# Performance work log

Hardware: AMD Instinct MI355X
Metric: run time of the kernel (lower is better)

The kernel has to match this reference:

```python
import jax, jax.numpy as jnp
import numpy as np

N, M, D, O = 16384, 4096, 256, 256

def setup_inputs() -> dict:
    key = jax.random.key(0)
    k1, k2, k3, k4, k5, k6, k7 = jax.random.split(key, 7)
    H_fine = jax.random.normal(k1, (N, D), dtype=jnp.float32)
    H_coarse = jax.random.normal(k2, (M, D), dtype=jnp.float32)
    inter_channel_adj = jax.random.randint(k3, (N, M), 0, 2).astype(jnp.float32)
    # attention = nn.Linear(2D, 1): weight vector [2D], bias scalar
    wa = jax.random.normal(k4, (2 * D,), dtype=jnp.float32) * (1.0 / np.sqrt(2 * D))
    ba = jax.random.normal(k5, (1,), dtype=jnp.float32) * 0.01
    # transform = nn.Linear(D, O), xavier_uniform weight
    lim = np.sqrt(6.0 / (D + O)).astype(np.float32)
    Wt = jax.random.uniform(k6, (O, D), minval=-lim, maxval=lim, dtype=jnp.float32)
    bt = jax.random.normal(k7, (O,), dtype=jnp.float32) * 0.01
    return {"H_fine": H_fine, "H_coarse": H_coarse,
            "inter_channel_adj": inter_channel_adj,
            "wa": wa, "ba": ba, "Wt": Wt, "bt": bt}

def reference(H_fine, H_coarse, inter_channel_adj, wa, ba, Wt, bt):
    d = H_fine.shape[-1]
    # additive attention: score_ij = [hf_i ; hc_j] . wa + b
    # = hf_i . wa[:d] + hc_j . wa[d:] + b  (avoids [N,M,2D] concat)
    sf = H_fine @ wa[:d]            # [N]
    sc = H_coarse @ wa[d:]          # [M]
    scores = sf[:, None] + sc[None, :] + ba[0]        # [N, M]
    masked = scores * inter_channel_adj               # [N, M]
    weights = jax.nn.softmax(masked, axis=-1)         # [N, M]
    attn_out = weights @ H_coarse                     # [N, D]
    attn_out = attn_out + H_fine                      # add_self=True
    out = attn_out @ Wt.T + bt                        # [N, O]
    return jax.nn.relu(out)
```

## Files before the change

### kernel.cpp

```cpp
#include <hip/hip_runtime.h>
#include <hip/hip_bf16.h>
#include <stdint.h>

#define N_ 16384
#define M_ 4096
#define D_ 256
#define O_ 256

#define WS_T    0
#define WS_U    65536
#define WS_R    81920
#define WS_LSUM 98304
#define WS_WTP  163840
#define WS_BP   294912
#define WS_ABM  2457600
#define WS_CP   10846208

typedef float  f32x4  __attribute__((ext_vector_type(4)));
typedef short  short8 __attribute__((ext_vector_type(8)));
typedef unsigned short ushortx4 __attribute__((ext_vector_type(4)));

__device__ __forceinline__ unsigned short f2bf(float f) {
  uint32_t u = __float_as_uint(f);
  u += 0x7FFFu + ((u >> 16) & 1u);
  return (unsigned short)(u >> 16);
}
__device__ __forceinline__ uint32_t cvtpk(float a, float b) {
  __hip_bfloat162 h = __float22bfloat162_rn(float2{a, b});
  uint32_t u;
  __builtin_memcpy(&u, &h, 4);
  return u;
}
__device__ __forceinline__ float bf2f(unsigned short v) {
  return __uint_as_float((uint32_t)v << 16);
}

__global__ __launch_bounds__(256) void rowdot_exp_kernel(
    const float* __restrict__ X, const float* __restrict__ w,
    const float* __restrict__ bias, float* __restrict__ outv) {
  int wv = threadIdx.x >> 6, lane = threadIdx.x & 63;
  int row = blockIdx.x * 4 + wv;
  const float4* x4 = (const float4*)(X + (size_t)row * D_);
  const float4* w4 = (const float4*)w;
  float4 xa = x4[lane], wa4 = w4[lane];
  float s = xa.x * wa4.x + xa.y * wa4.y + xa.z * wa4.z + xa.w * wa4.w;
#pragma unroll
  for (int off = 32; off > 0; off >>= 1) s += __shfl_xor(s, off);
  if (lane == 0) outv[row] = expf(s + (bias ? bias[0] : 0.0f));
}

__global__ __launch_bounds__(256) void hc_pack_kernel(
    const float* __restrict__ Hc, unsigned short* __restrict__ BP,
    float* __restrict__ R) {
  __shared__ float tile[64][65];
  __shared__ float red[4][64];
  int bk = blockIdx.x >> 2;
  int bc = blockIdx.x & 3;
  int k0 = bk * 64, col0 = bc * 64;
  int t = threadIdx.x;
  int lane = t & 63, wv = t >> 6;
  int m = lane & 15, q = lane >> 4;
  float colsum = 0.0f;
#pragma unroll
  for (int i = 0; i < 16; ++i) {
    int e = t + 256 * i;
    int kk = e >> 6, cc = e & 63;
    float v = Hc[(size_t)(k0 + kk) * D_ + col0 + cc];
    tile[kk][cc] = v;
    colsum += v;
  }
  red[wv][t & 63] = colsum;
  __syncthreads();
  if (t < 64)
    atomicAdd(&R[col0 + t], red[0][t] + red[1][t] + red[2][t] + red[3][t]);
#pragma unroll
  for (int t8 = 0; t8 < 2; ++t8) {
    int tile_id = t8 * 4 + wv;
    int sub = tile_id >> 2, g = tile_id & 3;
    int kgg = bk * 2 + sub;
    int cgg = bc * 4 + g;
    short8 v8;
#pragma unroll
    for (int j = 0; j < 8; ++j)
      v8[j] = (short)f2bf(tile[sub * 32 + q * 8 + j][g * 16 + m]);
    *(short8*)(BP + ((size_t)(kgg * 16 + cgg) * 64 + lane) * 8) = v8;
  }
}

__global__ __launch_bounds__(256) void wt_pack_kernel(
    const float* __restrict__ Wt, unsigned short* __restrict__ WtP) {
  int t = blockIdx.x * 256 + threadIdx.x;
  int lane = t & 63, cg = (t >> 6) & 15, kg = t >> 10;
  int m = lane & 15, q = lane >> 4;
  const float* src = Wt + (size_t)(cg * 16 + m) * D_ + kg * 32 + q * 8;
  float4 w0 = *(const float4*)src, w1 = *(const float4*)(src + 4);
  short8 v8;
  v8[0] = (short)f2bf(w0.x); v8[1] = (short)f2bf(w0.y);
  v8[2] = (short)f2bf(w0.z); v8[3] = (short)f2bf(w0.w);
  v8[4] = (short)f2bf(w1.x); v8[5] = (short)f2bf(w1.y);
  v8[6] = (short)f2bf(w1.z); v8[7] = (short)f2bf(w1.w);
  *(short8*)(WtP + (size_t)t * 8) = v8;
}

__global__ __launch_bounds__(256) void pack_bits_kernel(
    const float* __restrict__ adj, const float* __restrict__ tv,
    const float* __restrict__ uv, unsigned long long* __restrict__ ABM,
    float* __restrict__ Lsum) {
  __shared__ float u_lds[M_];
  int tid = threadIdx.x;
  int w = tid >> 6, lane = tid & 63;
  for (int i = tid; i < M_; i += 256) u_lds[i] = uv[i];
  __syncthreads();
  int r0 = (blockIdx.x * 4 + w) * 2;
  const float* arA = adj + (size_t)r0 * M_;
  const float* arB = arA + M_;
  float suA = 0.f, scA = 0.f, suB = 0.f, scB = 0.f;

  float a0 = arA[lane], a1 = arA[64 + lane], a2 = arA[128 + lane], a3 = arA[192 + lane];
  float b0 = arB[lane], b1 = arB[64 + lane], b2 = arB[128 + lane], b3 = arB[192 + lane];
#pragma unroll 1
  for (int i = 0; i < 16; ++i) {
    int k0 = i * 256;
    int k1 = (i + 1 < 16) ? k0 + 256 : 0;
    float na0 = arA[k1 + lane],       na1 = arA[k1 + 64 + lane];
    float na2 = arA[k1 + 128 + lane], na3 = arA[k1 + 192 + lane];
    float nb0 = arB[k1 + lane],       nb1 = arB[k1 + 64 + lane];
    float nb2 = arB[k1 + 128 + lane], nb3 = arB[k1 + 192 + lane];

    unsigned long long wA0 = __ballot(a0 != 0.0f), wA1 = __ballot(a1 != 0.0f);
    unsigned long long wA2 = __ballot(a2 != 0.0f), wA3 = __ballot(a3 != 0.0f);
    unsigned long long wB0 = __ballot(b0 != 0.0f), wB1 = __ballot(b1 != 0.0f);
    unsigned long long wB2 = __ballot(b2 != 0.0f), wB3 = __ballot(b3 != 0.0f);
    suA = fmaf(a0, u_lds[k0 + lane], suA);
    suA = fmaf(a1, u_lds[k0 + 64 + lane], suA);
    suA = fmaf(a2, u_lds[k0 + 128 + lane], suA);
    suA = fmaf(a3, u_lds[k0 + 192 + lane], suA);
    scA += (a0 + a1) + (a2 + a3);
    suB = fmaf(b0, u_lds[k0 + lane], suB);
    suB = fmaf(b1, u_lds[k0 + 64 + lane], suB);
    suB = fmaf(b2, u_lds[k0 + 128 + lane], suB);
    suB = fmaf(b3, u_lds[k0 + 192 + lane], suB);
    scB += (b0 + b1) + (b2 + b3);
    if (lane < 8) {
      int sel = lane & 3;
      unsigned long long vA = sel == 0 ? wA0 : sel == 1 ? wA1 : sel == 2 ? wA2 : wA3;
      unsigned long long vB = sel == 0 ? wB0 : sel == 1 ? wB1 : sel == 2 ? wB2 : wB3;
      int r = (lane < 4) ? r0 : r0 + 1;
      ABM[(size_t)r * 64 + i * 4 + sel] = (lane < 4) ? vA : vB;
    }
    a0 = na0; a1 = na1; a2 = na2; a3 = na3;
    b0 = nb0; b1 = nb1; b2 = nb2; b3 = nb3;
  }
#pragma unroll
  for (int off = 32; off > 0; off >>= 1) {
    suA += __shfl_xor(suA, off); scA += __shfl_xor(scA, off);
    suB += __shfl_xor(suB, off); scB += __shfl_xor(scB, off);
  }
  if (lane == 0) {
    Lsum[r0] = tv[r0] * suA - scA;
    Lsum[r0 + 1] = tv[r0 + 1] * suB - scB;
  }
}

__device__ __forceinline__ short8 frag_bits(uint32_t bits, float t,
                                            float4 u0, float4 u1) {
  float c[8];
  c[0] = fmaf(t, u0.x, -1.0f); c[1] = fmaf(t, u0.y, -1.0f);
  c[2] = fmaf(t, u0.z, -1.0f); c[3] = fmaf(t, u0.w, -1.0f);
  c[4] = fmaf(t, u1.x, -1.0f); c[5] = fmaf(t, u1.y, -1.0f);
  c[6] = fmaf(t, u1.z, -1.0f); c[7] = fmaf(t, u1.w, -1.0f);
  union { short8 s; uint32_t u[4]; } r;
#pragma unroll
  for (int p = 0; p < 4; ++p) {
    uint32_t mlo = 0u - ((bits >> (2 * p)) & 1u);
    uint32_t mhi = 0u - ((bits >> (2 * p + 1)) & 1u);
    r.u[p] = cvtpk(c[2 * p], c[2 * p + 1]) &
             ((mlo & 0x0000FFFFu) | (mhi & 0xFFFF0000u));
  }
  return r.s;
}

__global__ __launch_bounds__(1024, 4) void gemm_kernel(
    const unsigned int* __restrict__ ABM32, const unsigned short* __restrict__ BP,
    const float* __restrict__ tv, const float* __restrict__ uv,
    unsigned short* __restrict__ Cp) {
  __shared__ unsigned int bt2[64][129];
  __shared__ float u_lds[M_];
  int tid = threadIdx.x;
  int w = tid >> 6, lane = tid & 63;
  int q = lane >> 4, m = lane & 15;
  int colq = w >> 2, ksub = w & 3;
  int i0 = blockIdx.x * 64;

  const unsigned short* bbase = BP + (size_t)(colq * 4) * 512 + (size_t)lane * 8;
  int kg0 = ksub * 32;
  short8 curB[4];
#pragma unroll
  for (int n = 0; n < 4; ++n)
    curB[n] = *(const short8*)(bbase + ((size_t)kg0 * 16 + n) * 512);
  float t0 = tv[i0 + m], t1 = tv[i0 + 16 + m];
  float t2 = tv[i0 + 32 + m], t3 = tv[i0 + 48 + m];

  for (int i = tid; i < M_; i += 1024) u_lds[i] = uv[i];
  for (int p = tid; p < 8192; p += 1024) {
    int row = p >> 7, word = p & 127;
    bt2[row][word] = ABM32[(size_t)(i0 + row) * 128 + word];
  }

  f32x4 acc[4][4];
#pragma unroll
  for (int s = 0; s < 4; ++s)
#pragma unroll
    for (int n = 0; n < 4; ++n) acc[s][n] = (f32x4){0.f, 0.f, 0.f, 0.f};

  __syncthreads();

  for (int it = 0; it < 32; ++it) {
    int kg = kg0 + it;
    int kn = (it + 1 < 32) ? kg + 1 : kg0;
    short8 nB[4];
#pragma unroll
    for (int n = 0; n < 4; ++n)
      nB[n] = *(const short8*)(bbase + ((size_t)kn * 16 + n) * 512);

    float4 u0 = *(const float4*)&u_lds[kg * 32 + q * 8];
    float4 u1 = *(const float4*)&u_lds[kg * 32 + q * 8 + 4];
    uint32_t b0 = bt2[m][kg],      b1 = bt2[16 + m][kg];
    uint32_t b2 = bt2[32 + m][kg], b3 = bt2[48 + m][kg];
    int sh = q * 8;
    short8 af0 = frag_bits((b0 >> sh) & 0xffu, t0, u0, u1);
    short8 af1 = frag_bits((b1 >> sh) & 0xffu, t1, u0, u1);
    short8 af2 = frag_bits((b2 >> sh) & 0xffu, t2, u0, u1);
    short8 af3 = frag_bits((b3 >> sh) & 0xffu, t3, u0, u1);
#pragma unroll
    for (int n = 0; n < 4; ++n) {
      acc[0][n] = __builtin_amdgcn_mfma_f32_16x16x32_bf16(af0, curB[n], acc[0][n], 0, 0, 0);
      acc[1][n] = __builtin_amdgcn_mfma_f32_16x16x32_bf16(af1, curB[n], acc[1][n], 0, 0, 0);
      acc[2][n] = __builtin_amdgcn_mfma_f32_16x16x32_bf16(af2, curB[n], acc[2][n], 0, 0, 0);
      acc[3][n] = __builtin_amdgcn_mfma_f32_16x16x32_bf16(af3, curB[n], acc[3][n], 0, 0, 0);
    }
#pragma unroll
    for (int n = 0; n < 4; ++n) curB[n] = nB[n];
  }

  unsigned short* cpb = Cp + (size_t)ksub * N_ * D_;
#pragma unroll
  for (int s = 0; s < 4; ++s)
#pragma unroll
    for (int n = 0; n < 4; ++n) {
      int col = colq * 64 + n * 16 + m;
#pragma unroll
      for (int r = 0; r < 4; ++r) {
        size_t row = (size_t)i0 + s * 16 + q * 4 + r;
        cpb[row * D_ + col] = f2bf(acc[s][n][r]);
      }
    }
}

__global__ __launch_bounds__(256, 4) void epilogue_kernel(
    const unsigned short* __restrict__ Cp, const float* __restrict__ Lsum,
    const float* __restrict__ Rv, const float* __restrict__ Hf,
    const unsigned short* __restrict__ WtP, const float* __restrict__ bt,
    float* __restrict__ out) {
  __shared__ alignas(16) unsigned short attn[32][264];
  int tid = threadIdx.x;
  int w = tid >> 6, lane = tid & 63;
  int rtile = w & 1, chalf = w >> 1;
  int q = lane >> 4, m = lane & 15;
  int i0 = blockIdx.x * 32;

  float4 rv = *(const float4*)(Rv + lane * 4);
#pragma unroll
  for (int rr = 0; rr < 8; ++rr) {
    int r = w * 8 + rr;
    size_t row = (size_t)i0 + r;
    float invL = 1.0f / (Lsum[row] + (float)M_);
    ushortx4 c0 = *(const ushortx4*)(Cp + row * D_ + lane * 4);
    ushortx4 c1 = *(const ushortx4*)(Cp + ((size_t)N_ + row) * D_ + lane * 4);
    ushortx4 c2 = *(const ushortx4*)(Cp + ((size_t)2 * N_ + row) * D_ + lane * 4);
    ushortx4 c3 = *(const ushortx4*)(Cp + ((size_t)3 * N_ + row) * D_ + lane * 4);
    float4 hv = *(const float4*)(Hf + row * D_ + lane * 4);
    float s0 = (bf2f(c0[0]) + bf2f(c1[0])) + (bf2f(c2[0]) + bf2f(c3[0]));
    float s1 = (bf2f(c0[1]) + bf2f(c1[1])) + (bf2f(c2[1]) + bf2f(c3[1]));
    float s2 = (bf2f(c0[2]) + bf2f(c1[2])) + (bf2f(c2[2]) + bf2f(c3[2]));
    float s3 = (bf2f(c0[3]) + bf2f(c1[3])) + (bf2f(c2[3]) + bf2f(c3[3]));
    attn[r][lane * 4 + 0] = f2bf(fmaf(s0 + rv.x, invL, hv.x));
    attn[r][lane * 4 + 1] = f2bf(fmaf(s1 + rv.y, invL, hv.y));
    attn[r][lane * 4 + 2] = f2bf(fmaf(s2 + rv.z, invL, hv.z));
    attn[r][lane * 4 + 3] = f2bf(fmaf(s3 + rv.w, invL, hv.w));
  }
  __syncthreads();

  f32x4 facc[8];
#pragma unroll
  for (int n = 0; n < 8; ++n) facc[n] = (f32x4){0.f, 0.f, 0.f, 0.f};
  const unsigned short* wwave = WtP + (size_t)chalf * 4096 + (size_t)lane * 8;
#pragma unroll
  for (int kf = 0; kf < 8; ++kf) {
    short8 af = *(const short8*)&attn[rtile * 16 + m][kf * 32 + q * 8];
#pragma unroll
    for (int n = 0; n < 8; ++n) {
      short8 bf = *(const short8*)(wwave + ((size_t)kf * 16 + n) * 512);
      facc[n] = __builtin_amdgcn_mfma_f32_16x16x32_bf16(af, bf, facc[n], 0, 0, 0);
    }
  }
#pragma unroll
  for (int n = 0; n < 8; ++n) {
    int col = chalf * 128 + n * 16 + m;
    float b = bt[col];
#pragma unroll
    for (int r = 0; r < 4; ++r) {
      size_t row = (size_t)i0 + rtile * 16 + q * 4 + r;
      out[row * O_ + col] = fmaxf(facc[n][r] + b, 0.0f);
    }
  }
}

extern "C" void kernel_launch(void* const* d_in, const int* in_sizes, int n_in,
                              void* d_out, int out_size, void* d_ws, size_t ws_size,
                              hipStream_t stream) {
  const float* Hf  = (const float*)d_in[0];
  const float* Hc  = (const float*)d_in[1];
  const float* adj = (const float*)d_in[2];
  const float* wa  = (const float*)d_in[3];
  const float* ba  = (const float*)d_in[4];
  const float* Wt  = (const float*)d_in[5];
  const float* bt  = (const float*)d_in[6];
  float* out = (float*)d_out;

  char* ws = (char*)d_ws;
  float* tv   = (float*)(ws + WS_T);
  float* uv   = (float*)(ws + WS_U);
  float* Rv   = (float*)(ws + WS_R);
  float* Lsum = (float*)(ws + WS_LSUM);
  unsigned short* WtP = (unsigned short*)(ws + WS_WTP);
  unsigned short* BP  = (unsigned short*)(ws + WS_BP);
  unsigned long long* ABM = (unsigned long long*)(ws + WS_ABM);
  unsigned short* Cp  = (unsigned short*)(ws + WS_CP);

  hipMemsetAsync(Rv, 0, D_ * sizeof(float), stream);

  rowdot_exp_kernel<<<N_ / 4, 256, 0, stream>>>(Hf, wa, ba, tv);
  rowdot_exp_kernel<<<M_ / 4, 256, 0, stream>>>(Hc, wa + D_, nullptr, uv);
  hc_pack_kernel<<<256, 256, 0, stream>>>(Hc, BP, Rv);
  wt_pack_kernel<<<32, 256, 0, stream>>>(Wt, WtP);

  pack_bits_kernel<<<2048, 256, 0, stream>>>(adj, tv, uv, ABM, Lsum);
  gemm_kernel<<<N_ / 64, 1024, 0, stream>>>((const unsigned int*)ABM, BP, tv, uv, Cp);
  epilogue_kernel<<<N_ / 32, 256, 0, stream>>>(Cp, Lsum, Rv, Hf, WtP, bt, out);
}
```

Measured before the change: 487.8 us.

## Factor masked exp-weight GEMM into two bf16 GEMMs with pre-scaled coarse operand

The (t_i*u_j - 1)*mask weight is split algebraically into t_i*mask @ (u*Hc) plus -mask @ Hc. A-fragments are now built from bitmasks and constants alone, with no per-element FMA or bf16 conversion. Two packed B operands are precomputed in hc_pack, and the work split changes from 4 k-slices by 4 column quarters to 2 k-slices by 8 column groups. Partial sums are kept in fp32, so the epilogue reads only two partials. This doubles MFMA count and B-operand traffic in exchange for removing the VALU fragment build, and rounding t and u*Hc to bf16 separately may change accuracy.

```diff
diff --git a/kernel.cpp b/kernel.cpp
--- a/kernel.cpp
+++ b/kernel.cpp
@@ -12,13 +12,13 @@
 #define WS_R    81920
 #define WS_LSUM 98304
 #define WS_WTP  163840
-#define WS_BP   294912
-#define WS_ABM  2457600
-#define WS_CP   10846208
+#define WS_BP1  294912
+#define WS_BP2  2392064
+#define WS_ABM  4489216
+#define WS_CP   12877824
 
 typedef float  f32x4  __attribute__((ext_vector_type(4)));
 typedef short  short8 __attribute__((ext_vector_type(8)));
-typedef unsigned short ushortx4 __attribute__((ext_vector_type(4)));
 
 __device__ __forceinline__ unsigned short f2bf(float f) {
   uint32_t u = __float_as_uint(f);
@@ -30,9 +30,6 @@
   uint32_t u;
   __builtin_memcpy(&u, &h, 4);
   return u;
-}
-__device__ __forceinline__ float bf2f(unsigned short v) {
-  return __uint_as_float((uint32_t)v << 16);
 }
 
 __global__ __launch_bounds__(256) void rowdot_exp_kernel(
@@ -50,16 +47,19 @@
 }
 
 __global__ __launch_bounds__(256) void hc_pack_kernel(
-    const float* __restrict__ Hc, unsigned short* __restrict__ BP,
+    const float* __restrict__ Hc, const float* __restrict__ uv,
+    unsigned short* __restrict__ BP1, unsigned short* __restrict__ BP2,
     float* __restrict__ R) {
   __shared__ float tile[64][65];
   __shared__ float red[4][64];
+  __shared__ float u_tile[64];
   int bk = blockIdx.x >> 2;
   int bc = blockIdx.x & 3;
   int k0 = bk * 64, col0 = bc * 64;
   int t = threadIdx.x;
   int lane = t & 63, wv = t >> 6;
   int m = lane & 15, q = lane >> 4;
+  if (t < 64) u_tile[t] = uv[k0 + t];
   float colsum = 0.0f;
 #pragma unroll
   for (int i = 0; i < 16; ++i) {
@@ -79,11 +79,17 @@
     int sub = tile_id >> 2, g = tile_id & 3;
     int kgg = bk * 2 + sub;
     int cgg = bc * 4 + g;
-    short8 v8;
-#pragma unroll
-    for (int j = 0; j < 8; ++j)
-      v8[j] = (short)f2bf(tile[sub * 32 + q * 8 + j][g * 16 + m]);
-    *(short8*)(BP + ((size_t)(kgg * 16 + cgg) * 64 + lane) * 8) = v8;
+    short8 v1, v2;
+#pragma unroll
+    for (int j = 0; j < 8; ++j) {
+      int kk = sub * 32 + q * 8 + j;
+      float v = tile[kk][g * 16 + m];
+      v2[j] = (short)f2bf(v);
+      v1[j] = (short)f2bf(u_tile[kk] * v);
+    }
+    size_t off = ((size_t)(kgg * 16 + cgg) * 64 + lane) * 8;
+    *(short8*)(BP1 + off) = v1;
+    *(short8*)(BP2 + off) = v2;
   }
 }
 
@@ -162,103 +168,108 @@
   }
 }
 
-__device__ __forceinline__ short8 frag_bits(uint32_t bits, float t,
-                                            float4 u0, float4 u1) {
-  float c[8];
-  c[0] = fmaf(t, u0.x, -1.0f); c[1] = fmaf(t, u0.y, -1.0f);
-  c[2] = fmaf(t, u0.z, -1.0f); c[3] = fmaf(t, u0.w, -1.0f);
-  c[4] = fmaf(t, u1.x, -1.0f); c[5] = fmaf(t, u1.y, -1.0f);
-  c[6] = fmaf(t, u1.z, -1.0f); c[7] = fmaf(t, u1.w, -1.0f);
-  union { short8 s; uint32_t u[4]; } r;
+__device__ __forceinline__ void frag01(uint32_t bits, uint32_t tpk,
+                                       short8* a1, short8* a2) {
+  union { short8 s; uint32_t u[4]; } r1, r2;
 #pragma unroll
   for (int p = 0; p < 4; ++p) {
     uint32_t mlo = 0u - ((bits >> (2 * p)) & 1u);
     uint32_t mhi = 0u - ((bits >> (2 * p + 1)) & 1u);
-    r.u[p] = cvtpk(c[2 * p], c[2 * p + 1]) &
-             ((mlo & 0x0000FFFFu) | (mhi & 0xFFFF0000u));
-  }
-  return r.s;
+    uint32_t msk = (mlo & 0x0000FFFFu) | (mhi & 0xFFFF0000u);
+    r1.u[p] = tpk & msk;
+    r2.u[p] = 0xBF80BF80u & msk;
+  }
+  *a1 = r1.s; *a2 = r2.s;
 }
 
 __global__ __launch_bounds__(1024, 4) void gemm_kernel(
-    const unsigned int* __restrict__ ABM32, const unsigned short* __restrict__ BP,
-    const float* __restrict__ tv, const float* __restrict__ uv,
-    unsigned short* __restrict__ Cp) {
+    const unsigned int* __restrict__ ABM32, const unsigned short* __restrict__ BP1,
+    const unsigned short* __restrict__ BP2, const float* __restrict__ tv,
+    float* __restrict__ Cp) {
   __shared__ unsigned int bt2[64][129];
-  __shared__ float u_lds[M_];
   int tid = threadIdx.x;
   int w = tid >> 6, lane = tid & 63;
   int q = lane >> 4, m = lane & 15;
-  int colq = w >> 2, ksub = w & 3;
+  int colq = w & 7, ksub = w >> 3;
   int i0 = blockIdx.x * 64;
 
-  const unsigned short* bbase = BP + (size_t)(colq * 4) * 512 + (size_t)lane * 8;
-  int kg0 = ksub * 32;
-  short8 curB[4];
-#pragma unroll
-  for (int n = 0; n < 4; ++n)
-    curB[n] = *(const short8*)(bbase + ((size_t)kg0 * 16 + n) * 512);
-  float t0 = tv[i0 + m], t1 = tv[i0 + 16 + m];
+  float t0 = tv[i0 + m],      t1 = tv[i0 + 16 + m];
   float t2 = tv[i0 + 32 + m], t3 = tv[i0 + 48 + m];
-
-  for (int i = tid; i < M_; i += 1024) u_lds[i] = uv[i];
+  uint32_t tp0 = cvtpk(t0, t0), tp1 = cvtpk(t1, t1);
+  uint32_t tp2 = cvtpk(t2, t2), tp3 = cvtpk(t3, t3);
+
   for (int p = tid; p < 8192; p += 1024) {
     int row = p >> 7, word = p & 127;
     bt2[row][word] = ABM32[(size_t)(i0 + row) * 128 + word];
   }
 
-  f32x4 acc[4][4];
+  f32x4 acc[4][2];
 #pragma unroll
   for (int s = 0; s < 4; ++s)
 #pragma unroll
-    for (int n = 0; n < 4; ++n) acc[s][n] = (f32x4){0.f, 0.f, 0.f, 0.f};
+    for (int n = 0; n < 2; ++n) acc[s][n] = (f32x4){0.f, 0.f, 0.f, 0.f};
+
+  int kg0 = ksub * 64;
+  const unsigned short* b1p = BP1 + (size_t)(kg0 * 16 + colq * 2) * 512 + (size_t)lane * 8;
+  const unsigned short* b2p = BP2 + (size_t)(kg0 * 16 + colq * 2) * 512 + (size_t)lane * 8;
+  int sh = q * 8;
 
   __syncthreads();
 
-  for (int it = 0; it < 32; ++it) {
+#pragma unroll 2
+  for (int it = 0; it < 64; ++it) {
     int kg = kg0 + it;
-    int kn = (it + 1 < 32) ? kg + 1 : kg0;
-    short8 nB[4];
-#pragma unroll
-    for (int n = 0; n < 4; ++n)
-      nB[n] = *(const short8*)(bbase + ((size_t)kn * 16 + n) * 512);
-
-    float4 u0 = *(const float4*)&u_lds[kg * 32 + q * 8];
-    float4 u1 = *(const float4*)&u_lds[kg * 32 + q * 8 + 4];
-    uint32_t b0 = bt2[m][kg],      b1 = bt2[16 + m][kg];
-    uint32_t b2 = bt2[32 + m][kg], b3 = bt2[48 + m][kg];
-    int sh = q * 8;
-    short8 af0 = frag_bits((b0 >> sh) & 0xffu, t0, u0, u1);
-    short8 af1 = frag_bits((b1 >> sh) & 0xffu, t1, u0, u1);
-    short8 af2 = frag_bits((b2 >> sh) & 0xffu, t2, u0, u1);
-    short8 af3 = frag_bits((b3 >> sh) & 0xffu, t3, u0, u1);
-#pragma unroll
-    for (int n = 0; n < 4; ++n) {
-      acc[0][n] = __builtin_amdgcn_mfma_f32_16x16x32_bf16(af0, curB[n], acc[0][n], 0, 0, 0);
-      acc[1][n] = __builtin_amdgcn_mfma_f32_16x16x32_bf16(af1, curB[n], acc[1][n], 0, 0, 0);
-      acc[2][n] = __builtin_amdgcn_mfma_f32_16x16x32_bf16(af2, curB[n], acc[2][n], 0, 0, 0);
-      acc[3][n] = __builtin_amdgcn_mfma_f32_16x16x32_bf16(af3, curB[n], acc[3][n], 0, 0, 0);
-    }
-#pragma unroll
-    for (int n = 0; n < 4; ++n) curB[n] = nB[n];
-  }
-
-  unsigned short* cpb = Cp + (size_t)ksub * N_ * D_;
+    const unsigned short* b1k = b1p + (size_t)it * 8192;
+    const unsigned short* b2k = b2p + (size_t)it * 8192;
+    short8 B1a = *(const short8*)(b1k);
+    short8 B1b = *(const short8*)(b1k + 512);
+    short8 B2a = *(const short8*)(b2k);
+    short8 B2b = *(const short8*)(b2k + 512);
+
+    uint32_t w0 = (bt2[m][kg] >> sh) & 0xffu;
+    uint32_t w1 = (bt2[16 + m][kg] >> sh) & 0xffu;
+    uint32_t w2 = (bt2[32 + m][kg] >> sh) & 0xffu;
+    uint32_t w3 = (bt2[48 + m][kg] >> sh) & 0xffu;
+
+    short8 a1, a2;
+    frag01(w0, tp0, &a1, &a2);
+    acc[0][0] = __builtin_amdgcn_mfma_f32_16x16x32_bf16(a1, B1a, acc[0][0], 0, 0, 0);
+    acc[0][0] = __builtin_amdgcn_mfma_f32_16x16x32_bf16(a2, B2a, acc[0][0], 0, 0, 0);
+    acc[0][1] = __builtin_amdgcn_mfma_f32_16x16x32_bf16(a1, B1b, acc[0][1], 0, 0, 0);
+    acc[0][1] = __builtin_amdgcn_mfma_f32_16x16x32_bf16(a2, B2b, acc[0][1], 0, 0, 0);
+    frag01(w1, tp1, &a1, &a2);
+    acc[1][0] = __builtin_amdgcn_mfma_f32_16x16x32_bf16(a1, B1a, acc[1][0], 0, 0, 0);
+    acc[1][0] = __builtin_amdgcn_mfma_f32_16x16x32_bf16(a2, B2a, acc[1][0], 0, 0, 0);
+    acc[1][1] = __builtin_amdgcn_mfma_f32_16x16x32_bf16(a1, B1b, acc[1][1], 0, 0, 0);
+    acc[1][1] = __builtin_amdgcn_mfma_f32_16x16x32_bf16(a2, B2b, acc[1][1], 0, 0, 0);
+    frag01(w2, tp2, &a1, &a2);
+    acc[2][0] = __builtin_amdgcn_mfma_f32_16x16x32_bf16(a1, B1a, acc[2][0], 0, 0, 0);
+    acc[2][0] = __builtin_amdgcn_mfma_f32_16x16x32_bf16(a2, B2a, acc[2][0], 0, 0, 0);
+    acc[2][1] = __builtin_amdgcn_mfma_f32_16x16x32_bf16(a1, B1b, acc[2][1], 0, 0, 0);
+    acc[2][1] = __builtin_amdgcn_mfma_f32_16x16x32_bf16(a2, B2b, acc[2][1], 0, 0, 0);
+    frag01(w3, tp3, &a1, &a2);
+    acc[3][0] = __builtin_amdgcn_mfma_f32_16x16x32_bf16(a1, B1a, acc[3][0], 0, 0, 0);
+    acc[3][0] = __builtin_amdgcn_mfma_f32_16x16x32_bf16(a2, B2a, acc[3][0], 0, 0, 0);
+    acc[3][1] = __builtin_amdgcn_mfma_f32_16x16x32_bf16(a1, B1b, acc[3][1], 0, 0, 0);
+    acc[3][1] = __builtin_amdgcn_mfma_f32_16x16x32_bf16(a2, B2b, acc[3][1], 0, 0, 0);
+  }
+
+  float* cpb = Cp + (size_t)ksub * N_ * D_;
 #pragma unroll
   for (int s = 0; s < 4; ++s)
 #pragma unroll
-    for (int n = 0; n < 4; ++n) {
-      int col = colq * 64 + n * 16 + m;
+    for (int n = 0; n < 2; ++n) {
+      int col = (colq * 2 + n) * 16 + m;
 #pragma unroll
       for (int r = 0; r < 4; ++r) {
         size_t row = (size_t)i0 + s * 16 + q * 4 + r;
-        cpb[row * D_ + col] = f2bf(acc[s][n][r]);
+        cpb[row * D_ + col] = acc[s][n][r];
       }
     }
 }
 
 __global__ __launch_bounds__(256, 4) void epilogue_kernel(
-    const unsigned short* __restrict__ Cp, const float* __restrict__ Lsum,
+    const float* __restrict__ Cp, const float* __restrict__ Lsum,
     const float* __restrict__ Rv, const float* __restrict__ Hf,
     const unsigned short* __restrict__ WtP, const float* __restrict__ bt,
     float* __restrict__ out) {
@@ -275,19 +286,13 @@
     int r = w * 8 + rr;
     size_t row = (size_t)i0 + r;
     float invL = 1.0f / (Lsum[row] + (float)M_);
-    ushortx4 c0 = *(const ushortx4*)(Cp + row * D_ + lane * 4);
-    ushortx4 c1 = *(const ushortx4*)(Cp + ((size_t)N_ + row) * D_ + lane * 4);
-    ushortx4 c2 = *(const ushortx4*)(Cp + ((size_t)2 * N_ + row) * D_ + lane * 4);
-    ushortx4 c3 = *(const ushortx4*)(Cp + ((size_t)3 * N_ + row) * D_ + lane * 4);
+    float4 c0 = *(const float4*)(Cp + row * D_ + lane * 4);
+    float4 c1 = *(const float4*)(Cp + ((size_t)N_ + row) * D_ + lane * 4);
     float4 hv = *(const float4*)(Hf + row * D_ + lane * 4);
-    float s0 = (bf2f(c0[0]) + bf2f(c1[0])) + (bf2f(c2[0]) + bf2f(c3[0]));
-    float s1 = (bf2f(c0[1]) + bf2f(c1[1])) + (bf2f(c2[1]) + bf2f(c3[1]));
-    float s2 = (bf2f(c0[2]) + bf2f(c1[2])) + (bf2f(c2[2]) + bf2f(c3[2]));
-    float s3 = (bf2f(c0[3]) + bf2f(c1[3])) + (bf2f(c2[3]) + bf2f(c3[3]));
-    attn[r][lane * 4 + 0] = f2bf(fmaf(s0 + rv.x, invL, hv.x));
-    attn[r][lane * 4 + 1] = f2bf(fmaf(s1 + rv.y, invL, hv.y));
-    attn[r][lane * 4 + 2] = f2bf(fmaf(s2 + rv.z, invL, hv.z));
-    attn[r][lane * 4 + 3] = f2bf(fmaf(s3 + rv.w, invL, hv.w));
+    attn[r][lane * 4 + 0] = f2bf(fmaf(c0.x + c1.x + rv.x, invL, hv.x));
+    attn[r][lane * 4 + 1] = f2bf(fmaf(c0.y + c1.y + rv.y, invL, hv.y));
+    attn[r][lane * 4 + 2] = f2bf(fmaf(c0.z + c1.z + rv.z, invL, hv.z));
+    attn[r][lane * 4 + 3] = f2bf(fmaf(c0.w + c1.w + rv.w, invL, hv.w));
   }
   __syncthreads();
 
@@ -334,18 +339,19 @@
   float* Rv   = (float*)(ws + WS_R);
   float* Lsum = (float*)(ws + WS_LSUM);
   unsigned short* WtP = (unsigned short*)(ws + WS_WTP);
-  unsigned short* BP  = (unsigned short*)(ws + WS_BP);
+  unsigned short* BP1 = (unsigned short*)(ws + WS_BP1);
+  unsigned short* BP2 = (unsigned short*)(ws + WS_BP2);
   unsigned long long* ABM = (unsigned long long*)(ws + WS_ABM);
-  unsigned short* Cp  = (unsigned short*)(ws + WS_CP);
+  float* Cp = (float*)(ws + WS_CP);
 
   hipMemsetAsync(Rv, 0, D_ * sizeof(float), stream);
 
   rowdot_exp_kernel<<<N_ / 4, 256, 0, stream>>>(Hf, wa, ba, tv);
   rowdot_exp_kernel<<<M_ / 4, 256, 0, stream>>>(Hc, wa + D_, nullptr, uv);
-  hc_pack_kernel<<<256, 256, 0, stream>>>(Hc, BP, Rv);
+  hc_pack_kernel<<<256, 256, 0, stream>>>(Hc, uv, BP1, BP2, Rv);
   wt_pack_kernel<<<32, 256, 0, stream>>>(Wt, WtP);
 
   pack_bits_kernel<<<2048, 256, 0, stream>>>(adj, tv, uv, ABM, Lsum);
-  gemm_kernel<<<N_ / 64, 1024, 0, stream>>>((const unsigned int*)ABM, BP, tv, uv, Cp);
+  gemm_kernel<<<N_ / 64, 1024, 0, stream>>>((const unsigned int*)ABM, BP1, BP2, tv, Cp);
   epilogue_kernel<<<N_ / 32, 256, 0, stream>>>(Cp, Lsum, Rv, Hf, WtP, bt, out);
 }
```

New measurement: 509.8 us. +4.5%, slower.

## Fuse GEMM with epilogue via LDS split-K reduction and merge prep kernels

Applied to the files above, without the earlier changes.

Merges the four small preprocessing kernels into a single prep launch that dispatches on block index. Fuses the epilogue into the main GEMM kernel: the four k-split partial accumulators are reduced in shared memory instead of being written to and reread from a bf16 global buffer. The block then applies normalization, the residual and the second MFMA GEMM in place. This removes about 32 MB of intermediate global traffic and two launches, but raises LDS usage to about 115 KB per block and adds serialized reduction barriers, which may lower occupancy.

```diff
diff --git a/kernel.cpp b/kernel.cpp
--- a/kernel.cpp
+++ b/kernel.cpp
@@ -13,12 +13,10 @@
 #define WS_LSUM 98304
 #define WS_WTP  163840
 #define WS_BP   294912
-#define WS_ABM  2457600
-#define WS_CP   10846208
+#define WS_ABM  2392064
 
 typedef float  f32x4  __attribute__((ext_vector_type(4)));
 typedef short  short8 __attribute__((ext_vector_type(8)));
-typedef unsigned short ushortx4 __attribute__((ext_vector_type(4)));
 
 __device__ __forceinline__ unsigned short f2bf(float f) {
   uint32_t u = __float_as_uint(f);
@@ -31,75 +29,74 @@
   __builtin_memcpy(&u, &h, 4);
   return u;
 }
-__device__ __forceinline__ float bf2f(unsigned short v) {
-  return __uint_as_float((uint32_t)v << 16);
-}
-
-__global__ __launch_bounds__(256) void rowdot_exp_kernel(
-    const float* __restrict__ X, const float* __restrict__ w,
-    const float* __restrict__ bias, float* __restrict__ outv) {
-  int wv = threadIdx.x >> 6, lane = threadIdx.x & 63;
-  int row = blockIdx.x * 4 + wv;
-  const float4* x4 = (const float4*)(X + (size_t)row * D_);
-  const float4* w4 = (const float4*)w;
-  float4 xa = x4[lane], wa4 = w4[lane];
-  float s = xa.x * wa4.x + xa.y * wa4.y + xa.z * wa4.z + xa.w * wa4.w;
-#pragma unroll
-  for (int off = 32; off > 0; off >>= 1) s += __shfl_xor(s, off);
-  if (lane == 0) outv[row] = expf(s + (bias ? bias[0] : 0.0f));
-}
-
-__global__ __launch_bounds__(256) void hc_pack_kernel(
-    const float* __restrict__ Hc, unsigned short* __restrict__ BP,
-    float* __restrict__ R) {
+
+__global__ __launch_bounds__(256) void prep_kernel(
+    const float* __restrict__ Hf, const float* __restrict__ Hc,
+    const float* __restrict__ wa, const float* __restrict__ ba,
+    const float* __restrict__ Wt, float* __restrict__ tv,
+    float* __restrict__ uv, unsigned short* __restrict__ BP,
+    unsigned short* __restrict__ WtP, float* __restrict__ Rv) {
   __shared__ float tile[64][65];
   __shared__ float red[4][64];
-  int bk = blockIdx.x >> 2;
-  int bc = blockIdx.x & 3;
-  int k0 = bk * 64, col0 = bc * 64;
+  int b = blockIdx.x;
   int t = threadIdx.x;
-  int lane = t & 63, wv = t >> 6;
-  int m = lane & 15, q = lane >> 4;
-  float colsum = 0.0f;
-#pragma unroll
-  for (int i = 0; i < 16; ++i) {
-    int e = t + 256 * i;
-    int kk = e >> 6, cc = e & 63;
-    float v = Hc[(size_t)(k0 + kk) * D_ + col0 + cc];
-    tile[kk][cc] = v;
-    colsum += v;
-  }
-  red[wv][t & 63] = colsum;
-  __syncthreads();
-  if (t < 64)
-    atomicAdd(&R[col0 + t], red[0][t] + red[1][t] + red[2][t] + red[3][t]);
-#pragma unroll
-  for (int t8 = 0; t8 < 2; ++t8) {
-    int tile_id = t8 * 4 + wv;
-    int sub = tile_id >> 2, g = tile_id & 3;
-    int kgg = bk * 2 + sub;
-    int cgg = bc * 4 + g;
+  if (b < 5120) {
+    int wv = t >> 6, lane = t & 63;
+    const float* X; const float* w; const float* bias; float* outv; int row;
+    if (b < 4096) { X = Hf; w = wa;      bias = ba;      outv = tv; row = b * 4 + wv; }
+    else          { X = Hc; w = wa + D_; bias = nullptr; outv = uv; row = (b - 4096) * 4 + wv; }
+    const float4* x4 = (const float4*)(X + (size_t)row * D_);
+    const float4* w4 = (const float4*)w;
+    float4 xa = x4[lane], wa4 = w4[lane];
+    float s = xa.x * wa4.x + xa.y * wa4.y + xa.z * wa4.z + xa.w * wa4.w;
+#pragma unroll
+    for (int off = 32; off > 0; off >>= 1) s += __shfl_xor(s, off);
+    if (lane == 0) outv[row] = expf(s + (bias ? bias[0] : 0.0f));
+  } else if (b < 5376) {
+    int bb = b - 5120;
+    int bk = bb >> 2;
+    int bc = bb & 3;
+    int k0 = bk * 64, col0 = bc * 64;
+    int lane = t & 63, wv = t >> 6;
+    int m = lane & 15, q = lane >> 4;
+    float colsum = 0.0f;
+#pragma unroll
+    for (int i = 0; i < 16; ++i) {
+      int e = t + 256 * i;
+      int kk = e >> 6, cc = e & 63;
+      float v = Hc[(size_t)(k0 + kk) * D_ + col0 + cc];
+      tile[kk][cc] = v;
+      colsum += v;
+    }
+    red[wv][t & 63] = colsum;
+    __syncthreads();
+    if (t < 64)
+      atomicAdd(&Rv[col0 + t], red[0][t] + red[1][t] + red[2][t] + red[3][t]);
+#pragma unroll
+    for (int t8 = 0; t8 < 2; ++t8) {
+      int tile_id = t8 * 4 + wv;
+      int sub = tile_id >> 2, g = tile_id & 3;
+      int kgg = bk * 2 + sub;
+      int cgg = bc * 4 + g;
+      short8 v8;
+#pragma unroll
+      for (int j = 0; j < 8; ++j)
+        v8[j] = (short)f2bf(tile[sub * 32 + q * 8 + j][g * 16 + m]);
+      *(short8*)(BP + ((size_t)(kgg * 16 + cgg) * 64 + lane) * 8) = v8;
+    }
+  } else {
+    int tt = (b - 5376) * 256 + t;
+    int lane = tt & 63, cg = (tt >> 6) & 15, kg = tt >> 10;
+    int m = lane & 15, q = lane >> 4;
+    const float* src = Wt + (size_t)(cg * 16 + m) * D_ + kg * 32 + q * 8;
+    float4 w0 = *(const float4*)src, w1 = *(const float4*)(src + 4);
     short8 v8;
-#pragma unroll
-    for (int j = 0; j < 8; ++j)
-      v8[j] = (short)f2bf(tile[sub * 32 + q * 8 + j][g * 16 + m]);
-    *(short8*)(BP + ((size_t)(kgg * 16 + cgg) * 64 + lane) * 8) = v8;
-  }
-}
-
-__global__ __launch_bounds__(256) void wt_pack_kernel(
-    const float* __restrict__ Wt, unsigned short* __restrict__ WtP) {
-  int t = blockIdx.x * 256 + threadIdx.x;
-  int lane = t & 63, cg = (t >> 6) & 15, kg = t >> 10;
-  int m = lane & 15, q = lane >> 4;
-  const float* src = Wt + (size_t)(cg * 16 + m) * D_ + kg * 32 + q * 8;
-  float4 w0 = *(const float4*)src, w1 = *(const float4*)(src + 4);
-  short8 v8;
-  v8[0] = (short)f2bf(w0.x); v8[1] = (short)f2bf(w0.y);
-  v8[2] = (short)f2bf(w0.z); v8[3] = (short)f2bf(w0.w);
-  v8[4] = (short)f2bf(w1.x); v8[5] = (short)f2bf(w1.y);
-  v8[6] = (short)f2bf(w1.z); v8[7] = (short)f2bf(w1.w);
-  *(short8*)(WtP + (size_t)t * 8) = v8;
+    v8[0] = (short)f2bf(w0.x); v8[1] = (short)f2bf(w0.y);
+    v8[2] = (short)f2bf(w0.z); v8[3] = (short)f2bf(w0.w);
+    v8[4] = (short)f2bf(w1.x); v8[5] = (short)f2bf(w1.y);
+    v8[6] = (short)f2bf(w1.z); v8[7] = (short)f2bf(w1.w);
+    *(short8*)(WtP + (size_t)tt * 8) = v8;
+  }
 }
 
 __global__ __launch_bounds__(256) void pack_bits_kernel(
@@ -180,12 +177,18 @@
   return r.s;
 }
 
-__global__ __launch_bounds__(1024, 4) void gemm_kernel(
+__global__ __launch_bounds__(1024, 4) void mega_kernel(
     const unsigned int* __restrict__ ABM32, const unsigned short* __restrict__ BP,
     const float* __restrict__ tv, const float* __restrict__ uv,
-    unsigned short* __restrict__ Cp) {
-  __shared__ unsigned int bt2[64][129];
-  __shared__ float u_lds[M_];
+    const float* __restrict__ Lsum, const float* __restrict__ Rv,
+    const float* __restrict__ Hf, const unsigned short* __restrict__ WtP,
+    const float* __restrict__ bt, float* __restrict__ out) {
+  __shared__ __align__(16) char smem[114944];
+  unsigned int (*bt2)[129] = (unsigned int (*)[129])(smem);
+  float* u_lds = (float*)(smem + 33024);
+  float (*Cred)[256] = (float (*)[256])(smem + 49408);
+  unsigned short (*attn)[264] = (unsigned short (*)[264])(smem);
+
   int tid = threadIdx.x;
   int w = tid >> 6, lane = tid & 63;
   int q = lane >> 4, m = lane & 15;
@@ -243,75 +246,72 @@
     for (int n = 0; n < 4; ++n) curB[n] = nB[n];
   }
 
-  unsigned short* cpb = Cp + (size_t)ksub * N_ * D_;
-#pragma unroll
-  for (int s = 0; s < 4; ++s)
+#pragma unroll
+  for (int s4 = 0; s4 < 4; ++s4) {
+    if (ksub == s4) {
+#pragma unroll
+      for (int s = 0; s < 4; ++s)
+#pragma unroll
+        for (int n = 0; n < 4; ++n) {
+          int col = colq * 64 + n * 16 + m;
+#pragma unroll
+          for (int r = 0; r < 4; ++r) {
+            int rl = s * 16 + q * 4 + r;
+            if (s4 == 0) Cred[rl][col] = acc[s][n][r];
+            else         Cred[rl][col] += acc[s][n][r];
+          }
+        }
+    }
+    __syncthreads();
+  }
+
+  {
+    int row = tid >> 4;
+    int c0 = (tid & 15) * 16;
+    size_t grow = (size_t)i0 + row;
+    float invL = 1.0f / (Lsum[grow] + (float)M_);
+    const float* hfp = Hf + grow * D_ + c0;
+    const float* rvp = Rv + c0;
+    const float* crp = &Cred[row][c0];
+#pragma unroll
+    for (int g = 0; g < 4; ++g) {
+      float4 cv = *(const float4*)(crp + g * 4);
+      float4 rv = *(const float4*)(rvp + g * 4);
+      float4 hv = *(const float4*)(hfp + g * 4);
+      float v0 = fmaf(cv.x + rv.x, invL, hv.x);
+      float v1 = fmaf(cv.y + rv.y, invL, hv.y);
+      float v2 = fmaf(cv.z + rv.z, invL, hv.z);
+      float v3 = fmaf(cv.w + rv.w, invL, hv.w);
+      *(uint32_t*)&attn[row][c0 + g * 4]     = cvtpk(v0, v1);
+      *(uint32_t*)&attn[row][c0 + g * 4 + 2] = cvtpk(v2, v3);
+    }
+  }
+  __syncthreads();
+
+  {
+    int rt = w & 3, cq = w >> 2;
+    f32x4 facc[4];
+#pragma unroll
+    for (int n = 0; n < 4; ++n) facc[n] = (f32x4){0.f, 0.f, 0.f, 0.f};
+    const unsigned short* wwave = WtP + (size_t)(cq * 4) * 512 + (size_t)lane * 8;
+#pragma unroll
+    for (int kf = 0; kf < 8; ++kf) {
+      short8 af = *(const short8*)&attn[rt * 16 + m][kf * 32 + q * 8];
+#pragma unroll
+      for (int n = 0; n < 4; ++n) {
+        short8 bf = *(const short8*)(wwave + ((size_t)kf * 16 + n) * 512);
+        facc[n] = __builtin_amdgcn_mfma_f32_16x16x32_bf16(af, bf, facc[n], 0, 0, 0);
+      }
+    }
 #pragma unroll
     for (int n = 0; n < 4; ++n) {
-      int col = colq * 64 + n * 16 + m;
+      int col = cq * 64 + n * 16 + m;
+      float b = bt[col];
 #pragma unroll
       for (int r = 0; r < 4; ++r) {
-        size_t row = (size_t)i0 + s * 16 + q * 4 + r;
-        cpb[row * D_ + col] = f2bf(acc[s][n][r]);
+        size_t row = (size_t)i0 + rt * 16 + q * 4 + r;
+        out[row * O_ + col] = fmaxf(facc[n][r] + b, 0.0f);
       }
-    }
-}
-
-__global__ __launch_bounds__(256, 4) void epilogue_kernel(
-    const unsigned short* __restrict__ Cp, const float* __restrict__ Lsum,
-    const float* __restrict__ Rv, const float* __restrict__ Hf,
-    const unsigned short* __restrict__ WtP, const float* __restrict__ bt,
-    float* __restrict__ out) {
-  __shared__ alignas(16) unsigned short attn[32][264];
-  int tid = threadIdx.x;
-  int w = tid >> 6, lane = tid & 63;
-  int rtile = w & 1, chalf = w >> 1;
-  int q = lane >> 4, m = lane & 15;
-  int i0 = blockIdx.x * 32;
-
-  float4 rv = *(const float4*)(Rv + lane * 4);
-#pragma unroll
-  for (int rr = 0; rr < 8; ++rr) {
-    int r = w * 8 + rr;
-    size_t row = (size_t)i0 + r;
-    float invL = 1.0f / (Lsum[row] + (float)M_);
-    ushortx4 c0 = *(const ushortx4*)(Cp + row * D_ + lane * 4);
-    ushortx4 c1 = *(const ushortx4*)(Cp + ((size_t)N_ + row) * D_ + lane * 4);
-    ushortx4 c2 = *(const ushortx4*)(Cp + ((size_t)2 * N_ + row) * D_ + lane * 4);
-    ushortx4 c3 = *(const ushortx4*)(Cp + ((size_t)3 * N_ + row) * D_ + lane * 4);
-    float4 hv = *(const float4*)(Hf + row * D_ + lane * 4);
-    float s0 = (bf2f(c0[0]) + bf2f(c1[0])) + (bf2f(c2[0]) + bf2f(c3[0]));
-    float s1 = (bf2f(c0[1]) + bf2f(c1[1])) + (bf2f(c2[1]) + bf2f(c3[1]));
-    float s2 = (bf2f(c0[2]) + bf2f(c1[2])) + (bf2f(c2[2]) + bf2f(c3[2]));
-    float s3 = (bf2f(c0[3]) + bf2f(c1[3])) + (bf2f(c2[3]) + bf2f(c3[3]));
-    attn[r][lane * 4 + 0] = f2bf(fmaf(s0 + rv.x, invL, hv.x));
-    attn[r][lane * 4 + 1] = f2bf(fmaf(s1 + rv.y, invL, hv.y));
-    attn[r][lane * 4 + 2] = f2bf(fmaf(s2 + rv.z, invL, hv.z));
-    attn[r][lane * 4 + 3] = f2bf(fmaf(s3 + rv.w, invL, hv.w));
-  }
-  __syncthreads();
-
-  f32x4 facc[8];
-#pragma unroll
-  for (int n = 0; n < 8; ++n) facc[n] = (f32x4){0.f, 0.f, 0.f, 0.f};
-  const unsigned short* wwave = WtP + (size_t)chalf * 4096 + (size_t)lane * 8;
-#pragma unroll
-  for (int kf = 0; kf < 8; ++kf) {
-    short8 af = *(const short8*)&attn[rtile * 16 + m][kf * 32 + q * 8];
-#pragma unroll
-    for (int n = 0; n < 8; ++n) {
-      short8 bf = *(const short8*)(wwave + ((size_t)kf * 16 + n) * 512);
-      facc[n] = __builtin_amdgcn_mfma_f32_16x16x32_bf16(af, bf, facc[n], 0, 0, 0);
-    }
-  }
-#pragma unroll
-  for (int n = 0; n < 8; ++n) {
-    int col = chalf * 128 + n * 16 + m;
-    float b = bt[col];
-#pragma unroll
-    for (int r = 0; r < 4; ++r) {
-      size_t row = (size_t)i0 + rtile * 16 + q * 4 + r;
-      out[row * O_ + col] = fmaxf(facc[n][r] + b, 0.0f);
     }
   }
 }
@@ -336,16 +336,11 @@
   unsigned short* WtP = (unsigned short*)(ws + WS_WTP);
   unsigned short* BP  = (unsigned short*)(ws + WS_BP);
   unsigned long long* ABM = (unsigned long long*)(ws + WS_ABM);
-  unsigned short* Cp  = (unsigned short*)(ws + WS_CP);
 
   hipMemsetAsync(Rv, 0, D_ * sizeof(float), stream);
 
-  rowdot_exp_kernel<<<N_ / 4, 256, 0, stream>>>(Hf, wa, ba, tv);
-  rowdot_exp_kernel<<<M_ / 4, 256, 0, stream>>>(Hc, wa + D_, nullptr, uv);
-  hc_pack_kernel<<<256, 256, 0, stream>>>(Hc, BP, Rv);
-  wt_pack_kernel<<<32, 256, 0, stream>>>(Wt, WtP);
-
+  prep_kernel<<<5408, 256, 0, stream>>>(Hf, Hc, wa, ba, Wt, tv, uv, BP, WtP, Rv);
   pack_bits_kernel<<<2048, 256, 0, stream>>>(adj, tv, uv, ABM, Lsum);
-  gemm_kernel<<<N_ / 64, 1024, 0, stream>>>((const unsigned int*)ABM, BP, tv, uv, Cp);
-  epilogue_kernel<<<N_ / 32, 256, 0, stream>>>(Cp, Lsum, Rv, Hf, WtP, bt, out);
-}
+  mega_kernel<<<256, 1024, 0, stream>>>((const unsigned int*)ABM, BP, tv, uv,
+                                        Lsum, Rv, Hf, WtP, bt, out);
+}
```

Result: faster. 470.6 us (-3.5%).
